# Optimization experiments

Hardware: AMD Instinct MI355X
Metric: run time of the kernel (lower is better)

Reference implementation:

```python
import jax, jax.numpy as jnp
import numpy as np

B, T, N, D = 64, 12, 207, 128
H, ORDER = 8, 2
HID = 2 * D  # mlp_ratio = 2


def _ln(x, g, b, eps=1e-5):
    m = x.mean(-1, keepdims=True)
    v = ((x - m) ** 2).mean(-1, keepdims=True)
    return (x - m) * jax.lax.rsqrt(v + eps) * g + b


def _l2norm(t, eps=1e-12):
    # matches torch.nn.functional.normalize(dim=-1)
    n = jnp.sqrt((t * t).sum(-1, keepdims=True))
    return t / jnp.maximum(n, eps)


def _fast_attn(q, k, v):
    # q, k, v: (B2, L, H, Dh); Performer-style linear attention from FastAttentionLayer.fast_attention
    q = _l2norm(q)
    k = _l2norm(k)
    L = q.shape[1]
    kvs = jnp.einsum('blhm,blhd->bhmd', k, v)
    num = jnp.einsum('bnhm,bhmd->bnhd', q, kvs) + L * v
    ks_sum = k.sum(axis=1)  # (B2, H, Dh)
    den = jnp.einsum('bnhm,bhm->bnh', q, ks_sum)[..., None] + L
    return num / jnp.maximum(den, 1e-5)


def _fast_layer(x, qkv_w, out_w, out_b):
    # x: (B, T, N, D). qkv_bias=False (mask arg), kernel=3 -> out_proj: Linear(2D, D)
    b, t, n, d = x.shape
    dh = d // H
    qkv = x @ qkv_w.T  # (B, T, N, 3D)
    q, k, v = jnp.split(qkv, 3, axis=-1)
    # spatial pass: attend over the N nodes for each (b, t)
    out_s = _fast_attn(q.reshape(b * t, n, H, dh),
                       k.reshape(b * t, n, H, dh),
                       v.reshape(b * t, n, H, dh)).reshape(b, t, n, d)
    # temporal pass: attend over the T steps for each (b, n)
    qt = q.transpose(0, 2, 1, 3).reshape(b * n, t, H, dh)
    kt = k.transpose(0, 2, 1, 3).reshape(b * n, t, H, dh)
    vt = v.transpose(0, 2, 1, 3).reshape(b * n, t, H, dh)
    out_t = _fast_attn(qt, kt, vt).reshape(b, n, t, d).transpose(0, 2, 1, 3)
    return jnp.concatenate([out_s, out_t], -1) @ out_w.T + out_b


def _forward(x, graph, qkv_w, out_w, out_b, pw_w, pw_b,
             fc1_w, fc1_b, fc2_w, fc2_b, ln1_g, ln1_b, ln2_g, ln2_b):
    # GraphPropagate: x_list = [x, graph @ x, ...] (Ks = ORDER hops)
    xs = [x]
    xk = x
    for _ in range(ORDER - 1):
        xk = jnp.einsum('thi,btij->bthj', graph, xk)
        xs.append(xk)
    # per-hop fast attention + zero-init pointwise branch, summed over hops
    agg = jnp.zeros_like(x)
    for i in range(ORDER):
        agg = agg + _fast_layer(xs[i], qkv_w[i], out_w[i], out_b[i]) + xs[i] @ pw_w[i].T + pw_b[i]
    h = _ln(x + agg, ln1_g, ln1_b)
    ff = jax.nn.relu(h @ fc1_w.T + fc1_b) @ fc2_w.T + fc2_b
    return _ln(h + ff, ln2_g, ln2_b)


def setup_inputs() -> dict:
    key = jax.random.key(0)
    ks = jax.random.split(key, 8)
    s = 0.02
    return {
        'x': jax.random.normal(ks[0], (B, T, N, D), jnp.float32),
        'graph': jax.random.uniform(ks[1], (T, N, N), jnp.float32) / N,
        'qkv_w': jax.random.normal(ks[2], (ORDER, 3 * D, D), jnp.float32) * s,
        'out_w': jax.random.normal(ks[3], (ORDER, D, 2 * D), jnp.float32) * s,
        'out_b': jnp.zeros((ORDER, D), jnp.float32),
        'pw_w': jax.random.normal(ks[4], (ORDER, D, D), jnp.float32) * s,
        'pw_b': jnp.zeros((ORDER, D), jnp.float32),
        'fc1_w': jax.random.normal(ks[5], (HID, D), jnp.float32) * s,
        'fc1_b': jnp.zeros((HID,), jnp.float32),
        'fc2_w': jax.random.normal(ks[6], (D, HID), jnp.float32) * s,
        'fc2_b': jnp.zeros((D,), jnp.float32),
        'ln1_g': jnp.ones((D,), jnp.float32),
        'ln1_b': jnp.zeros((D,), jnp.float32),
        'ln2_g': jnp.ones((D,), jnp.float32),
        'ln2_b': jnp.zeros((D,), jnp.float32),
    }


def reference(x, graph, qkv_w, out_w, out_b, pw_w, pw_b,
              fc1_w, fc1_b, fc2_w, fc2_b, ln1_g, ln1_b, ln2_g, ln2_b):
    return _forward(x, graph, qkv_w, out_w, out_b, pw_w, pw_b,
                    fc1_w, fc1_b, fc2_w, fc2_b, ln1_g, ln1_b, ln2_g, ln2_b)
```

## Files before the change

### kernel.cpp

```cpp
#include <hip/hip_runtime.h>
#include <hip/hip_bf16.h>

#define BB 64
#define TT 12
#define NN 207
#define DD 128
#define HH 8
#define DH 16
#define MROWS (BB*TT*NN)
#define KPAD 224
#define AW 768
#define CHB 32
#define CROWS (CHB*TT*NN)

typedef __bf16 bf16x8 __attribute__((ext_vector_type(8)));
typedef __bf16 bf16x4 __attribute__((ext_vector_type(4)));
typedef float  f32x4  __attribute__((ext_vector_type(4)));

__device__ inline float  b2f(__bf16 v){ return (float)v; }
__device__ inline __bf16 f2b(float v){ return (__bf16)v; }
__device__ inline bf16x8 ldfrag(const __bf16* p){ return *reinterpret_cast<const bf16x8*>(p); }

__device__ inline void gload_lds16(const __bf16* g, __bf16* l){
    __builtin_amdgcn_global_load_lds(
        (const __attribute__((address_space(1))) void*)(g),
        (__attribute__((address_space(3))) void*)(l), 16, 0, 0);
}
__device__ inline int swz(int r){ return (r ^ (r>>2)) & 3; }
__device__ inline int pkey(int c){ return (c + (c>>2)) & 3; }

__global__ __launch_bounds__(256) void xcopy_kernel(const float* __restrict__ x, __bf16* __restrict__ abuf)
{
    int nt = gridDim.x*256;
    for (int gIdx = blockIdx.x*256 + threadIdx.x; gIdx < MROWS*16; gIdx += nt) {
        int row = gIdx >> 4, c8 = (gIdx & 15)*8;
        const float* s = x + (size_t)row*DD + c8;
        f32x4 a = *reinterpret_cast<const f32x4*>(s);
        f32x4 b = *reinterpret_cast<const f32x4*>(s+4);
        bf16x8 r;
        #pragma unroll
        for (int i=0;i<4;i++){ r[i] = f2b(a[i]); r[i+4] = f2b(b[i]); }
        *reinterpret_cast<bf16x8*>(abuf + (size_t)row*AW + c8) = r;
    }
}

__global__ __launch_bounds__(256) void prep_misc_kernel(
    const float* __restrict__ graph, const float* __restrict__ qkv_w,
    const float* __restrict__ out_w, const float* __restrict__ out_b,
    const float* __restrict__ pw_w,  const float* __restrict__ pw_b,
    const float* __restrict__ fc1_w, const float* __restrict__ fc2_w,
    __bf16* __restrict__ gpad, __bf16* __restrict__ qkv_wb, __bf16* __restrict__ wcomb,
    __bf16* __restrict__ fc1_wb, __bf16* __restrict__ fc2_wb, float* __restrict__ bias_comb)
{
    int nt = gridDim.x*256;
    int tid = blockIdx.x*256 + threadIdx.x;
    for (int i = tid; i < TT*NN*KPAD; i += nt) {
        int k = i % KPAD, r = i / KPAD;
        gpad[i] = (k < NN) ? f2b(graph[(size_t)r*NN + k]) : f2b(0.f);
    }
    for (int i = tid; i < 2*3*DD*DD; i += nt) qkv_wb[i] = f2b(qkv_w[i]);
    for (int i = tid; i < DD*AW; i += nt) {
        int c = i / AW, j = i % AW;
        float v;
        if      (j < 128) v = pw_w[c*128 + j];
        else if (j < 256) v = pw_w[128*128 + c*128 + (j-128)];
        else if (j < 512) v = out_w[c*256 + (j-256)];
        else              v = out_w[128*256 + c*256 + (j-512)];
        wcomb[i] = f2b(v);
    }
    for (int i = tid; i < 2*DD*DD; i += nt) fc1_wb[i] = f2b(fc1_w[i]);
    for (int i = tid; i < 2*DD*DD; i += nt) fc2_wb[i] = f2b(fc2_w[i]);
    for (int i = tid; i < DD; i += nt)
        bias_comb[i] = pw_b[i] + pw_b[128+i] + out_b[i] + out_b[128+i];
}

__global__ __launch_bounds__(256) void propagate_kernel(const __bf16* __restrict__ gp,
    __bf16* __restrict__ abuf)
{
    int bt   = blockIdx.x;
    int t    = bt % TT;
    int tile = blockIdx.y;
    int lane = threadIdx.x & 63, w = threadIdx.x >> 6;
    int lhi = lane >> 4, llo = lane & 15;
    __shared__ __attribute__((aligned(16))) __bf16 XT[DD][40];
    const __bf16* xbt  = abuf + (size_t)bt*NN*AW;
    const __bf16* grow = gp + (size_t)t*NN*KPAD;
    int rowbase = tile*64 + w*16;
    f32x4 acc[8];
    #pragma unroll
    for (int i=0;i<8;i++) acc[i] = (f32x4){0.f,0.f,0.f,0.f};
    int arow = rowbase + llo; if (arow > NN-1) arow = NN-1;
    for (int k0=0; k0<KPAD; k0+=32) {
        __syncthreads();
        for (int kl = (threadIdx.x>>7); kl < 32; kl += 2) {
            int kk = k0 + kl, c = threadIdx.x & 127;
            __bf16 xb = (kk < NN) ? xbt[(size_t)kk*AW + c] : f2b(0.f);
            XT[c][(((kl>>3) ^ pkey(c))<<3) | (kl&7)] = xb;
        }
        __syncthreads();
        bf16x8 a = ldfrag(grow + (size_t)arow*KPAD + k0 + lhi*8);
        #pragma unroll
        for (int cf=0;cf<8;cf++){
            int row = cf*16+llo;
            bf16x8 b = *reinterpret_cast<const bf16x8*>(&XT[row][(lhi ^ pkey(row))<<3]);
            acc[cf] = __builtin_amdgcn_mfma_f32_16x16x32_bf16(a, b, acc[cf], 0,0,0);
        }
    }
    #pragma unroll
    for (int e=0;e<4;e++){
        int row = rowbase + lhi*4 + e;
        if (row < NN) {
            #pragma unroll
            for (int cf=0;cf<8;cf++)
                abuf[((size_t)bt*NN + row)*AW + DD + cf*16 + llo] = f2b(acc[cf][e]);
        }
    }
}

template<int MODE, bool RELU>
__global__ __launch_bounds__(512) void gemm_kernel(const __bf16* __restrict__ A, size_t lda,
    const __bf16* __restrict__ W, const float* __restrict__ bias,
    void* out, size_t ldc, int K, int mend,
    const __bf16* __restrict__ resid, size_t ldr,
    const float* __restrict__ lng, const float* __restrict__ lnb)
{
    __shared__ __attribute__((aligned(16))) __bf16 lds[3][12288];
    int w = threadIdx.x >> 6, lane = threadIdx.x & 63;
    int lhi = lane >> 4, llo = lane & 15;
    size_t row0 = (size_t)blockIdx.x*256;
    int col0 = blockIdx.y*128;
    int nt = K >> 5;

    int sA0 = (w*2+0)*64 + lane, sA1 = (w*2+1)*64 + lane, sW = w*64 + lane;
    int rA0 = sA0>>2, uA0 = sA0&3, rA1 = sA1>>2, uA1 = sA1&3, rW = sW>>2, uW = sW&3;
    long gr0 = (long)row0 + rA0; if (gr0 >= mend) gr0 = mend-1;
    long gr1 = (long)row0 + rA1; if (gr1 >= mend) gr1 = mend-1;
    const __bf16* gA0 = A + (size_t)gr0*lda + ((uA0 ^ swz(rA0))<<3);
    const __bf16* gA1 = A + (size_t)gr1*lda + ((uA1 ^ swz(rA1))<<3);
    const __bf16* gW  = W + (size_t)(col0 + rW)*K + ((uW ^ swz(rW))<<3);
    __bf16* base0 = &lds[0][0];

    int aoff[2], woff[8];
    #pragma unroll
    for (int rt=0;rt<2;rt++){
        int rl = w*32 + rt*16 + llo;
        aoff[rt] = rl*32 + ((lhi ^ swz(rl))<<3);
    }
    #pragma unroll
    for (int cf=0;cf<8;cf++){
        int wr = cf*16 + llo;
        woff[cf] = 8192 + wr*32 + ((lhi ^ swz(wr))<<3);
    }

    f32x4 acc[2][8];
    #pragma unroll
    for (int i=0;i<2;i++)
        #pragma unroll
        for (int j=0;j<8;j++) acc[i][j] = (f32x4){0.f,0.f,0.f,0.f};

    #define STAGE(buf, tt) { int k0 = (tt)<<5; __bf16* Lw = base0 + (buf)*12288;           \
        gload_lds16(gA0 + k0, Lw + (w*2+0)*512);                                           \
        gload_lds16(gA1 + k0, Lw + (w*2+1)*512);                                           \
        gload_lds16(gW  + k0, Lw + 8192 + w*512); }

    STAGE(0,0); STAGE(1,1); STAGE(2,2);

    int cur = 0;
    for (int t = 0; t < nt; ++t) {
        if (t <= nt-3)      asm volatile("s_waitcnt vmcnt(6)" ::: "memory");
        else if (t == nt-2) asm volatile("s_waitcnt vmcnt(3)" ::: "memory");
        else                asm volatile("s_waitcnt vmcnt(0)" ::: "memory");
        __builtin_amdgcn_s_barrier();
        __builtin_amdgcn_sched_barrier(0);
        const __bf16* Lb = base0 + cur*12288;
        bf16x8 a[2], b[8];
        #pragma unroll
        for (int rt=0;rt<2;rt++) a[rt] = *reinterpret_cast<const bf16x8*>(&Lb[aoff[rt]]);
        #pragma unroll
        for (int cf=0;cf<8;cf++)  b[cf] = *reinterpret_cast<const bf16x8*>(&Lb[woff[cf]]);
        asm volatile("s_waitcnt lgkmcnt(0)" ::: "memory");
        __builtin_amdgcn_sched_barrier(0);
        __builtin_amdgcn_s_barrier();
        if (t+3 < nt) STAGE(cur, t+3);
        #pragma unroll
        for (int rt=0;rt<2;rt++)
            #pragma unroll
            for (int cf=0;cf<8;cf++)
                acc[rt][cf] = __builtin_amdgcn_mfma_f32_16x16x32_bf16(a[rt], b[cf], acc[rt][cf], 0,0,0);
        cur = (cur == 2) ? 0 : cur + 1;
    }
    #undef STAGE

    float bv[8];
    #pragma unroll
    for (int cf=0;cf<8;cf++) bv[cf] = bias ? bias[col0 + cf*16 + llo] : 0.f;

    if (MODE == 0) {
        #pragma unroll
        for (int rt=0;rt<2;rt++) {
            #pragma unroll
            for (int e=0;e<4;e++) {
                size_t row = row0 + (size_t)w*32 + rt*16 + lhi*4 + e;
                if ((long)row >= mend) continue;
                #pragma unroll
                for (int cf=0;cf<8;cf++) {
                    float v = acc[rt][cf][e] + bv[cf];
                    if (RELU) v = fmaxf(v, 0.f);
                    ((__bf16*)out)[row*ldc + col0 + cf*16 + llo] = f2b(v);
                }
            }
        }
    } else {
        float g8[8], b8[8];
        #pragma unroll
        for (int cf=0;cf<8;cf++){ int c = cf*16 + llo; g8[cf] = lng[c]; b8[cf] = lnb[c]; }
        #pragma unroll
        for (int rt=0;rt<2;rt++) {
            #pragma unroll
            for (int e=0;e<4;e++) {
                size_t row = row0 + (size_t)w*32 + rt*16 + lhi*4 + e;
                if ((long)row >= mend) continue;
                float vals[8], s = 0.f, ss = 0.f;
                #pragma unroll
                for (int cf=0;cf<8;cf++) {
                    int c = cf*16 + llo;
                    float r = b2f(resid[row*ldr + c]);
                    float v = acc[rt][cf][e] + bv[cf] + r;
                    vals[cf] = v; s += v; ss += v*v;
                }
                #pragma unroll
                for (int o=1;o<16;o<<=1){ s += __shfl_xor(s,o,64); ss += __shfl_xor(ss,o,64); }
                float mean = s * (1.f/DD);
                float var  = ss * (1.f/DD) - mean*mean;
                float rs   = rsqrtf(var + 1e-5f);
                #pragma unroll
                for (int cf=0;cf<8;cf++) {
                    float v = (vals[cf]-mean)*rs*g8[cf] + b8[cf];
                    ((__bf16*)out)[row*ldc + cf*16 + llo] = f2b(v);
                }
            }
        }
    }
}

template<bool RELU>
__global__ __launch_bounds__(256) void sgemm_k128(const __bf16* __restrict__ A, size_t lda,
    const __bf16* __restrict__ W, const float* __restrict__ bias,
    __bf16* __restrict__ out, size_t ldc, int ngroups)
{
    __shared__ __attribute__((aligned(16))) __bf16 lds[12][2048];
    int w = threadIdx.x >> 6, lane = threadIdx.x & 63;
    int lhi = lane >> 4, llo = lane & 15;
    int col0 = blockIdx.y*128;

    bf16x8 wf[4][8];
    #pragma unroll
    for (int ks=0;ks<4;ks++)
        #pragma unroll
        for (int cf=0;cf<8;cf++)
            wf[ks][cf] = ldfrag(W + (size_t)(col0 + cf*16 + llo)*128 + ks*32 + lhi*8);

    f32x4 bvv[8];
    #pragma unroll
    for (int cf=0;cf<8;cf++){
        if (bias) bvv[cf] = *reinterpret_cast<const f32x4*>(bias + col0 + cf*16 + lhi*4);
        else      bvv[cf] = (f32x4){0.f,0.f,0.f,0.f};
    }

    size_t gsrc[4];
    #pragma unroll
    for (int j=0;j<4;j++){
        int r = j*4 + lhi;
        int u = llo ^ r;
        gsrc[j] = (size_t)r*lda + (size_t)u*8;
    }
    int aoff[4];
    #pragma unroll
    for (int ks=0;ks<4;ks++) aoff[ks] = llo*128 + (((ks<<2)|lhi) ^ llo)*8;

    int gw = blockIdx.x*4 + w, stride = gridDim.x*4;
    int n = (gw < ngroups) ? ((ngroups-1-gw)/stride + 1) : 0;
    __bf16* slab0 = &lds[w*3][0];

    #define SSTAGE(i) { size_t rbase = (size_t)(gw + (size_t)(i)*stride)*16*lda;           \
        __bf16* L = slab0 + ((i)%3)*2048;                                                  \
        gload_lds16(A + rbase + gsrc[0], L);                                               \
        gload_lds16(A + rbase + gsrc[1], L + 512);                                         \
        gload_lds16(A + rbase + gsrc[2], L + 1024);                                        \
        gload_lds16(A + rbase + gsrc[3], L + 1536); }

    if (n > 0) SSTAGE(0);
    if (n > 1) SSTAGE(1);

    for (int i = 0; i < n; ++i) {
        int kept = ((i+1 < n) ? 4 : 0) + ((i >= 2) ? 16 : i*8);
        if      (kept >= 20) asm volatile("s_waitcnt vmcnt(20)" ::: "memory");
        else if (kept == 16) asm volatile("s_waitcnt vmcnt(16)" ::: "memory");
        else if (kept == 12) asm volatile("s_waitcnt vmcnt(12)" ::: "memory");
        else if (kept == 8)  asm volatile("s_waitcnt vmcnt(8)"  ::: "memory");
        else if (kept == 4)  asm volatile("s_waitcnt vmcnt(4)"  ::: "memory");
        else                 asm volatile("s_waitcnt vmcnt(0)"  ::: "memory");

        const __bf16* Ls = slab0 + (i%3)*2048;
        bf16x8 a[4];
        #pragma unroll
        for (int ks=0;ks<4;ks++) a[ks] = *reinterpret_cast<const bf16x8*>(&Ls[aoff[ks]]);

        if (i+2 < n) SSTAGE(i+2);

        f32x4 acc[8];
        #pragma unroll
        for (int cf=0;cf<8;cf++) acc[cf] = (f32x4){0.f,0.f,0.f,0.f};
        #pragma unroll
        for (int ks=0;ks<4;ks++)
            #pragma unroll
            for (int cf=0;cf<8;cf++)
                acc[cf] = __builtin_amdgcn_mfma_f32_16x16x32_bf16(wf[ks][cf], a[ks], acc[cf], 0,0,0);

        size_t grow = (size_t)(gw + (size_t)i*stride)*16 + llo;
        #pragma unroll
        for (int cf=0;cf<8;cf++){
            bf16x4 o;
            #pragma unroll
            for (int e=0;e<4;e++){
                float v = acc[cf][e] + bvv[cf][e];
                if (RELU) v = fmaxf(v, 0.f);
                o[e] = f2b(v);
            }
            *reinterpret_cast<bf16x4*>(out + grow*ldc + col0 + cf*16 + lhi*4) = o;
        }
    }
    #undef SSTAGE
}

__global__ __launch_bounds__(256) void ffn_kernel(const __bf16* __restrict__ h,
    const __bf16* __restrict__ w1, const float* __restrict__ b1,
    const __bf16* __restrict__ w2, const float* __restrict__ b2,
    const float* __restrict__ lng, const float* __restrict__ lnb,
    float* __restrict__ dout)
{
    __shared__ __attribute__((aligned(16))) __bf16 hring[2][4096];
    __shared__ __attribute__((aligned(16))) __bf16 f1b[8192];
    __shared__ float fl2[2][32][4][2];
    int w = threadIdx.x >> 6, lane = threadIdx.x & 63;
    int lhi = lane >> 4, llo = lane & 15;
    size_t row0 = (size_t)blockIdx.x * 64;

    size_t gsrc[2]; int ldst[2];
    #pragma unroll
    for (int j=0;j<2;j++){
        int i = w*64 + lane + 256*j;
        int r = i >> 4, u = i & 15;
        gsrc[j] = (size_t)r*AW + ((u ^ (r & 15)) << 3);
        ldst[j] = (w*64 + 256*j) * 8;
    }
    #define FSTAGE(slot, g) { const __bf16* src = h + (row0 + (size_t)(g)*32)*AW;          \
        gload_lds16(src + gsrc[0], &hring[slot][0] + ldst[0]);                             \
        gload_lds16(src + gsrc[1], &hring[slot][0] + ldst[1]); }

    f32x4 b1v[4], b2v[2], gv[2], bt2[2];
    #pragma unroll
    for (int c4=0;c4<4;c4++) b1v[c4] = *reinterpret_cast<const f32x4*>(b1 + w*64 + c4*16 + lhi*4);
    #pragma unroll
    for (int c2=0;c2<2;c2++){
        b2v[c2] = *reinterpret_cast<const f32x4*>(b2  + w*32 + c2*16 + lhi*4);
        gv[c2]  = *reinterpret_cast<const f32x4*>(lng + w*32 + c2*16 + lhi*4);
        bt2[c2] = *reinterpret_cast<const f32x4*>(lnb + w*32 + c2*16 + lhi*4);
    }

    FSTAGE(0,0); FSTAGE(1,1);

    for (int g = 0; g < 2; ++g) {
        if (g == 0) asm volatile("s_waitcnt vmcnt(2)" ::: "memory");
        else        asm volatile("s_waitcnt vmcnt(0)" ::: "memory");
        __builtin_amdgcn_s_barrier();
        __builtin_amdgcn_sched_barrier(0);
        const __bf16* Hs = &hring[g][0];

        bf16x8 hb[2][4];
        bf16x4 hres[2][2];
        #pragma unroll
        for (int rf=0;rf<2;rf++){
            int r = rf*16 + llo;
            #pragma unroll
            for (int ks=0;ks<4;ks++)
                hb[rf][ks] = *reinterpret_cast<const bf16x8*>(Hs + r*128 + (((ks*4+lhi) ^ llo) << 3));
            #pragma unroll
            for (int cf=0;cf<2;cf++){
                int unit = w*4 + cf*2 + (lhi>>1);
                hres[cf][rf] = *reinterpret_cast<const bf16x4*>(Hs + r*128 + ((unit ^ llo) << 3) + (lhi & 1)*4);
            }
        }
        asm volatile("s_waitcnt lgkmcnt(0)" ::: "memory");
        __builtin_amdgcn_sched_barrier(0);

        f32x4 acc1[4][2];
        #pragma unroll
        for (int i=0;i<4;i++){ acc1[i][0] = (f32x4){0,0,0,0}; acc1[i][1] = (f32x4){0,0,0,0}; }
        #pragma unroll
        for (int ks=0;ks<4;ks++){
            #pragma unroll
            for (int cf2=0;cf2<4;cf2++){
                bf16x8 wfr = ldfrag(w1 + (size_t)(w*64 + cf2*16 + llo)*128 + ks*32 + lhi*8);
                #pragma unroll
                for (int rf=0;rf<2;rf++)
                    acc1[cf2][rf] = __builtin_amdgcn_mfma_f32_16x16x32_bf16(wfr, hb[rf][ks], acc1[cf2][rf], 0,0,0);
            }
        }
        #pragma unroll
        for (int rf=0;rf<2;rf++){
            int r = rf*16 + llo;
            #pragma unroll
            for (int cf2=0;cf2<4;cf2++){
                bf16x4 o;
                #pragma unroll
                for (int e=0;e<4;e++) o[e] = f2b(fmaxf(acc1[cf2][rf][e] + b1v[cf2][e], 0.f));
                int unit = w*8 + cf2*2 + (lhi>>1);
                *reinterpret_cast<bf16x4*>(&f1b[r*256 + ((unit ^ r) << 3) + (lhi&1)*4]) = o;
            }
        }
        asm volatile("s_waitcnt lgkmcnt(0)" ::: "memory");
        __builtin_amdgcn_sched_barrier(0);
        __builtin_amdgcn_s_barrier();

        f32x4 acc2[2][2];
        acc2[0][0]=(f32x4){0,0,0,0}; acc2[0][1]=(f32x4){0,0,0,0};
        acc2[1][0]=(f32x4){0,0,0,0}; acc2[1][1]=(f32x4){0,0,0,0};
        #pragma unroll
        for (int ks2=0;ks2<8;ks2++){
            bf16x8 fb[2];
            #pragma unroll
            for (int rf=0;rf<2;rf++){
                int r = rf*16 + llo;
                fb[rf] = *reinterpret_cast<const bf16x8*>(&f1b[r*256 + (((ks2*4+lhi) ^ r) << 3)]);
            }
            #pragma unroll
            for (int cf=0;cf<2;cf++){
                bf16x8 wfr = ldfrag(w2 + (size_t)(w*32 + cf*16 + llo)*256 + ks2*32 + lhi*8);
                #pragma unroll
                for (int rf=0;rf<2;rf++)
                    acc2[cf][rf] = __builtin_amdgcn_mfma_f32_16x16x32_bf16(wfr, fb[rf], acc2[cf][rf], 0,0,0);
            }
        }

        float vals[2][2][4]; float s[2] = {0.f,0.f}, ss[2] = {0.f,0.f};
        #pragma unroll
        for (int rf=0;rf<2;rf++)
            #pragma unroll
            for (int cf=0;cf<2;cf++)
                #pragma unroll
                for (int e=0;e<4;e++){
                    float v = acc2[cf][rf][e] + b2v[cf][e] + b2f(hres[cf][rf][e]);
                    vals[rf][cf][e] = v; s[rf] += v; ss[rf] += v*v;
                }
        #pragma unroll
        for (int rf=0;rf<2;rf++){
            s[rf]  += __shfl_xor(s[rf],16,64);  s[rf]  += __shfl_xor(s[rf],32,64);
            ss[rf] += __shfl_xor(ss[rf],16,64); ss[rf] += __shfl_xor(ss[rf],32,64);
            if (lhi == 0){ fl2[g][rf*16+llo][w][0] = s[rf]; fl2[g][rf*16+llo][w][1] = ss[rf]; }
        }
        asm volatile("s_waitcnt lgkmcnt(0)" ::: "memory");
        __builtin_amdgcn_s_barrier();
        #pragma unroll
        for (int rf=0;rf<2;rf++){
            int r = rf*16 + llo;
            float S  = fl2[g][r][0][0]+fl2[g][r][1][0]+fl2[g][r][2][0]+fl2[g][r][3][0];
            float SS = fl2[g][r][0][1]+fl2[g][r][1][1]+fl2[g][r][2][1]+fl2[g][r][3][1];
            float mean = S*(1.f/DD), var = SS*(1.f/DD)-mean*mean, rs = rsqrtf(var+1e-5f);
            size_t grow = row0 + (size_t)g*32 + r;
            #pragma unroll
            for (int cf=0;cf<2;cf++){
                f32x4 o;
                #pragma unroll
                for (int e=0;e<4;e++) o[e] = (vals[rf][cf][e]-mean)*rs*gv[cf][e] + bt2[cf][e];
                *reinterpret_cast<f32x4*>(dout + grow*DD + w*32 + cf*16 + lhi*4) = o;
            }
        }
        if (g == 0) __builtin_amdgcn_s_barrier();
    }
    #undef FSTAGE
}

#define ACH 32
#define SBLKS (CHB*TT*4)
__global__ __launch_bounds__(256) void attn_st_kernel(const __bf16* __restrict__ qkv,
    __bf16* __restrict__ outs, __bf16* __restrict__ outt)
{
    __shared__ __attribute__((aligned(16))) char smem[44032];
    int tid = threadIdx.x;
    int bx = blockIdx.x;

    if (bx < SBLKS) {
        int bt = bx >> 2, g = bx & 3;
        const __bf16* base = qkv + (size_t)bt*NN*384 + g*32;
        __bf16 (*qbuf)[40] = (__bf16(*)[40])(smem);
        __bf16 (*vbuf)[40] = (__bf16(*)[40])(smem + 17920);
        __bf16 (*kbuf)[40] = (__bf16(*)[40])(smem + 35840);
        float (*flk)[16][17] = (float(*)[16][17])(smem + 38400);
        float (*fls)[16]     = (float(*)[16])(smem + 42752);
        int wave = tid >> 6, lane = tid & 63;
        int h2 = tid >> 7;
        int dd = tid & 15;
        int oct = ((tid >> 4) & 3) | ((wave & 1) << 2);
        float kvs_col[16]; float ks = 0.f;
        #pragma unroll
        for (int m=0;m<16;m++) kvs_col[m] = 0.f;

        for (int c0 = 0; c0 < NN; c0 += ACH) {
            __syncthreads();
            for (int i = tid; i < ACH*12; i += 256) {
                int r = i/12, u = i%12, seg = u>>2, uu = u&3;
                int nn = c0 + r;
                bf16x8 v8 = (bf16x8){};
                if (nn < NN) v8 = *reinterpret_cast<const bf16x8*>(base + (size_t)nn*384 + seg*128 + uu*8);
                if      (seg == 0) *reinterpret_cast<bf16x8*>(&qbuf[nn][uu*8]) = v8;
                else if (seg == 1) *reinterpret_cast<bf16x8*>(&kbuf[r][uu*8])  = v8;
                else               *reinterpret_cast<bf16x8*>(&vbuf[nn][uu*8]) = v8;
            }
            __syncthreads();
            #pragma unroll
            for (int j=0;j<4;j++){
                int r = oct + 8*j; int nn = c0 + r;
                if (nn >= NN) continue;
                bf16x8 k0 = *reinterpret_cast<const bf16x8*>(&kbuf[r][h2*16]);
                bf16x8 k1 = *reinterpret_cast<const bf16x8*>(&kbuf[r][h2*16+8]);
                float sk = 0.f;
                #pragma unroll
                for (int m=0;m<8;m++){
                    float a0=b2f(k0[m]), a1=b2f(k1[m]); sk += a0*a0 + a1*a1;
                }
                float iv = 1.f/fmaxf(sqrtf(sk), 1e-12f);
                float vv  = b2f(vbuf[nn][h2*16+dd]);
                float kdd = b2f(kbuf[r][h2*16+dd]);
                float t2 = iv*vv;
                #pragma unroll
                for (int m=0;m<8;m++){
                    kvs_col[m]   += b2f(k0[m])*t2;
                    kvs_col[m+8] += b2f(k1[m])*t2;
                }
                ks += kdd*iv;
            }
        }
        #pragma unroll
        for (int m=0;m<16;m++){
            kvs_col[m] += __shfl_xor(kvs_col[m], 16, 64);
            kvs_col[m] += __shfl_xor(kvs_col[m], 32, 64);
        }
        ks += __shfl_xor(ks, 16, 64);
        ks += __shfl_xor(ks, 32, 64);
        if (lane < 16){
            #pragma unroll
            for (int m=0;m<16;m++) flk[wave][m][lane] = kvs_col[m];
            fls[wave][lane] = ks;
        }
        __syncthreads();
        float ksr[16];
        #pragma unroll
        for (int m=0;m<16;m++){
            kvs_col[m] += flk[wave^1][m][dd];
            ksr[m] = fls[h2*2][m] + fls[h2*2+1][m];
        }
        for (int nn = oct; nn < NN; nn += 8) {
            bf16x8 q0 = *reinterpret_cast<const bf16x8*>(&qbuf[nn][h2*16]);
            bf16x8 q1 = *reinterpret_cast<const bf16x8*>(&qbuf[nn][h2*16+8]);
            float sq = 0.f, num = 0.f, den = 0.f;
            #pragma unroll
            for (int m=0;m<8;m++){
                float qm0 = b2f(q0[m]), qm1 = b2f(q1[m]);
                sq  += qm0*qm0 + qm1*qm1;
                num += qm0*kvs_col[m] + qm1*kvs_col[m+8];
                den += qm0*ksr[m]     + qm1*ksr[m+8];
            }
            float iq = 1.f/fmaxf(sqrtf(sq), 1e-12f);
            float vv = b2f(vbuf[nn][h2*16+dd]);
            float o = (num*iq + (float)NN*vv) / fmaxf(den*iq + (float)NN, 1e-5f);
            outs[((size_t)bt*NN + nn)*AW + g*32 + h2*16 + dd] = f2b(o);
        }
    } else {
        int tix = bx - SBLKS;
        int b = tix / 104;
        int nn0 = (tix % 104) * 2;
        __bf16 (*rows)[2][384] = (__bf16(*)[2][384])(smem);
        float (*invq)[TT][8]  = (float(*)[TT][8])(smem + 18432);
        float (*invk2)[TT][8] = (float(*)[TT][8])(smem + 19200);
        for (int i = tid; i < TT*2*48; i += 256) {
            int t = i / 96, rem = i % 96;
            int nl = rem / 48, g = rem % 48;
            int nn = nn0 + nl;
            bf16x8 v8 = (bf16x8){};
            if (nn < NN) v8 = *reinterpret_cast<const bf16x8*>(qkv + ((size_t)(b*TT+t)*NN + nn)*384 + g*8);
            *reinterpret_cast<bf16x8*>(&rows[t][nl][g*8]) = v8;
        }
        __syncthreads();
        if (tid < 192) {
            int hh = tid & 7, t = (tid >> 3) % TT, nl = tid / 96;
            bf16x8 q0 = *reinterpret_cast<const bf16x8*>(&rows[t][nl][hh*16]);
            bf16x8 q1 = *reinterpret_cast<const bf16x8*>(&rows[t][nl][hh*16+8]);
            bf16x8 k0 = *reinterpret_cast<const bf16x8*>(&rows[t][nl][128+hh*16]);
            bf16x8 k1 = *reinterpret_cast<const bf16x8*>(&rows[t][nl][128+hh*16+8]);
            float sq = 0.f, sk = 0.f;
            #pragma unroll
            for (int m=0;m<8;m++){
                float a0=b2f(q0[m]), a1=b2f(q1[m]); sq += a0*a0 + a1*a1;
                float c0v=b2f(k0[m]), c1=b2f(k1[m]); sk += c0v*c0v + c1*c1;
            }
            invq[nl][t][hh]  = 1.f/fmaxf(sqrtf(sq), 1e-12f);
            invk2[nl][t][hh] = 1.f/fmaxf(sqrtf(sk), 1e-12f);
        }
        __syncthreads();
        int dd = tid & 15, h = (tid >> 4) & 7, nl = tid >> 7;
        int nn = nn0 + nl;
        float kvs_col[16], ksum[16];
        #pragma unroll
        for (int m=0;m<16;m++){ kvs_col[m]=0.f; ksum[m]=0.f; }
        #pragma unroll
        for (int t=0;t<TT;t++){
            float iv = invk2[nl][t][h];
            bf16x8 k0 = *reinterpret_cast<const bf16x8*>(&rows[t][nl][128+h*16]);
            bf16x8 k1 = *reinterpret_cast<const bf16x8*>(&rows[t][nl][128+h*16+8]);
            float vv = b2f(rows[t][nl][256+h*16+dd]);
            float t2 = iv*vv;
            #pragma unroll
            for (int m=0;m<8;m++){
                float km0 = b2f(k0[m]), km1 = b2f(k1[m]);
                kvs_col[m]   += km0*t2;  ksum[m]   += km0*iv;
                kvs_col[m+8] += km1*t2;  ksum[m+8] += km1*iv;
            }
        }
        #pragma unroll
        for (int t=0;t<TT;t++){
            float iq = invq[nl][t][h];
            bf16x8 q0 = *reinterpret_cast<const bf16x8*>(&rows[t][nl][h*16]);
            bf16x8 q1 = *reinterpret_cast<const bf16x8*>(&rows[t][nl][h*16+8]);
            float num = 0.f, den = 0.f;
            #pragma unroll
            for (int m=0;m<8;m++){
                float qm0 = b2f(q0[m]), qm1 = b2f(q1[m]);
                num += qm0*kvs_col[m]  + qm1*kvs_col[m+8];
                den += qm0*ksum[m]     + qm1*ksum[m+8];
            }
            float vv = b2f(rows[t][nl][256+h*16+dd]);
            float o = (num*iq + (float)TT*vv) / fmaxf(den*iq + (float)TT, 1e-5f);
            if (nn < NN)
                outt[((size_t)(b*TT+t)*NN + nn)*AW + h*16 + dd] = f2b(o);
        }
    }
}

extern "C" void kernel_launch(void* const* d_in, const int* in_sizes, int n_in,
                              void* d_out, int out_size, void* d_ws, size_t ws_size,
                              hipStream_t stream)
{
    const float* x     = (const float*)d_in[0];
    const float* graph = (const float*)d_in[1];
    const float* qkv_w = (const float*)d_in[2];
    const float* out_w = (const float*)d_in[3];
    const float* out_b = (const float*)d_in[4];
    const float* pw_w  = (const float*)d_in[5];
    const float* pw_b  = (const float*)d_in[6];
    const float* fc1_w = (const float*)d_in[7];
    const float* fc1_b = (const float*)d_in[8];
    const float* fc2_w = (const float*)d_in[9];
    const float* fc2_b = (const float*)d_in[10];
    const float* ln1g  = (const float*)d_in[11];
    const float* ln1b  = (const float*)d_in[12];
    const float* ln2g  = (const float*)d_in[13];
    const float* ln2b  = (const float*)d_in[14];
    (void)in_sizes; (void)n_in; (void)out_size; (void)ws_size;

    char* ws = (char*)d_ws;
    size_t off = 0;
    __bf16* abuf = (__bf16*)(ws + off); off += (size_t)MROWS*AW*2;
    __bf16* qkvc = (__bf16*)(ws + off); off += (size_t)CROWS*3*DD*2;
    __bf16* gpad = (__bf16*)(ws + off); off += (size_t)TT*NN*KPAD*2;
    __bf16* qkv_wb = (__bf16*)(ws + off); off += (size_t)2*3*DD*DD*2;
    __bf16* wcomb  = (__bf16*)(ws + off); off += (size_t)DD*AW*2;
    __bf16* fc1_wb = (__bf16*)(ws + off); off += (size_t)2*DD*DD*2;
    __bf16* fc2_wb = (__bf16*)(ws + off); off += (size_t)2*DD*DD*2;
    float*  bias_comb = (float*)(ws + off); off += DD*4;

    dim3 blk(256), blk512(512);

    xcopy_kernel<<<dim3(4096), blk, 0, stream>>>(x, abuf);
    prep_misc_kernel<<<dim3(1024), blk, 0, stream>>>(graph, qkv_w, out_w, out_b, pw_w, pw_b,
        fc1_w, fc2_w, gpad, qkv_wb, wcomb, fc1_wb, fc2_wb, bias_comb);
    propagate_kernel<<<dim3(BB*TT, 4), blk, 0, stream>>>(gpad, abuf);

    for (int hop = 0; hop < 2; ++hop) {
        for (int c = 0; c < BB/CHB; ++c) {
            size_t rowoff = (size_t)c*CROWS;
            sgemm_k128<false><<<dim3(170, 3), blk, 0, stream>>>(
                abuf + rowoff*AW + hop*DD, (size_t)AW, qkv_wb + (size_t)hop*3*DD*DD, nullptr,
                qkvc, (size_t)(3*DD), CROWS/16);
            attn_st_kernel<<<dim3(SBLKS + CHB*104), blk, 0, stream>>>(
                qkvc, abuf + rowoff*AW + 256 + hop*256, abuf + rowoff*AW + 384 + hop*256);
        }
    }

    gemm_kernel<3,false><<<dim3(MROWS/256, 1), blk512, 0, stream>>>(
        abuf, (size_t)AW, wcomb, bias_comb, (void*)abuf, (size_t)AW, AW, MROWS,
        abuf, (size_t)AW, ln1g, ln1b);
    ffn_kernel<<<dim3(MROWS/64), blk, 0, stream>>>(
        abuf, fc1_wb, fc1_b, fc2_wb, fc2_b, ln2g, ln2b, (float*)d_out);
}
```

Before: 817.8 us.

## Use MFMA for spatial linear-attention KV and output computation

Rewrites the spatial branch of the attention kernel so that K^T V, the k-sum and the q·KV / q·ksum products run as bf16 MFMA instructions instead of scalar FMA loops. Normalized K and V are staged transposed in shared memory per chunk, and the two waves per head alternate chunks and combine their partial sums afterwards. The change adds shared-memory use, an extra barrier per chunk, and rounds KV and ksum to bf16 before the output MFMA, which costs some precision.

```diff
diff --git a/kernel.cpp b/kernel.cpp
--- a/kernel.cpp
+++ b/kernel.cpp
@@ -16,6 +16,7 @@
 typedef __bf16 bf16x8 __attribute__((ext_vector_type(8)));
 typedef __bf16 bf16x4 __attribute__((ext_vector_type(4)));
 typedef float  f32x4  __attribute__((ext_vector_type(4)));
+typedef short  s16x4  __attribute__((ext_vector_type(4)));
 
 __device__ inline float  b2f(__bf16 v){ return (float)v; }
 __device__ inline __bf16 f2b(float v){ return (__bf16)v; }
@@ -486,7 +487,7 @@
 __global__ __launch_bounds__(256) void attn_st_kernel(const __bf16* __restrict__ qkv,
     __bf16* __restrict__ outs, __bf16* __restrict__ outt)
 {
-    __shared__ __attribute__((aligned(16))) char smem[44032];
+    __shared__ __attribute__((aligned(16))) char smem[49664];
     int tid = threadIdx.x;
     int bx = blockIdx.x;
 
@@ -496,17 +497,24 @@
         __bf16 (*qbuf)[40] = (__bf16(*)[40])(smem);
         __bf16 (*vbuf)[40] = (__bf16(*)[40])(smem + 17920);
         __bf16 (*kbuf)[40] = (__bf16(*)[40])(smem + 35840);
-        float (*flk)[16][17] = (float(*)[16][17])(smem + 38400);
-        float (*fls)[16]     = (float(*)[16])(smem + 42752);
+        __bf16 (*khT)[40]  = (__bf16(*)[40])(smem + 38400);
+        __bf16 (*vT)[40]   = (__bf16(*)[40])(smem + 40960);
+        float  (*iqt)[224] = (float(*)[224])(smem + 43520);
+        float*  kvp        = (float*)(smem + 45312);
+        float*  ksp        = (float*)(smem + 49408);
         int wave = tid >> 6, lane = tid & 63;
-        int h2 = tid >> 7;
-        int dd = tid & 15;
-        int oct = ((tid >> 4) & 3) | ((wave & 1) << 2);
-        float kvs_col[16]; float ks = 0.f;
-        #pragma unroll
-        for (int m=0;m<16;m++) kvs_col[m] = 0.f;
-
-        for (int c0 = 0; c0 < NN; c0 += ACH) {
+        int lhi = lane >> 4, llo = lane & 15;
+        int h = wave >> 1;
+        int r8 = tid >> 3, i8 = tid & 7;
+        int thead = i8 >> 2, tm4 = (i8 & 3) * 4;
+
+        f32x4 kvs = (f32x4){0,0,0,0}, ksm = (f32x4){0,0,0,0};
+        bf16x8 ones8;
+        #pragma unroll
+        for (int j=0;j<8;j++) ones8[j] = f2b(1.0f);
+
+        for (int c = 0; c < 7; ++c) {
+            int c0 = c*32;
             __syncthreads();
             for (int i = tid; i < ACH*12; i += 256) {
                 int r = i/12, u = i%12, seg = u>>2, uu = u&3;
@@ -518,63 +526,65 @@
                 else               *reinterpret_cast<bf16x8*>(&vbuf[nn][uu*8]) = v8;
             }
             __syncthreads();
-            #pragma unroll
-            for (int j=0;j<4;j++){
-                int r = oct + 8*j; int nn = c0 + r;
-                if (nn >= NN) continue;
-                bf16x8 k0 = *reinterpret_cast<const bf16x8*>(&kbuf[r][h2*16]);
-                bf16x8 k1 = *reinterpret_cast<const bf16x8*>(&kbuf[r][h2*16+8]);
-                float sk = 0.f;
-                #pragma unroll
-                for (int m=0;m<8;m++){
-                    float a0=b2f(k0[m]), a1=b2f(k1[m]); sk += a0*a0 + a1*a1;
+            {
+                int r = r8, nn = c0 + r8;
+                float kv[4], vv[4];
+                float sk = 0.f, sq = 0.f;
+                #pragma unroll
+                for (int j=0;j<4;j++){
+                    kv[j] = b2f(kbuf[r][thead*16 + tm4 + j]); sk += kv[j]*kv[j];
+                    float qv = b2f(qbuf[nn][thead*16 + tm4 + j]); sq += qv*qv;
+                    vv[j] = b2f(vbuf[nn][thead*16 + tm4 + j]);
                 }
+                sk += __shfl_xor(sk,1,64); sk += __shfl_xor(sk,2,64);
+                sq += __shfl_xor(sq,1,64); sq += __shfl_xor(sq,2,64);
                 float iv = 1.f/fmaxf(sqrtf(sk), 1e-12f);
-                float vv  = b2f(vbuf[nn][h2*16+dd]);
-                float kdd = b2f(kbuf[r][h2*16+dd]);
-                float t2 = iv*vv;
-                #pragma unroll
-                for (int m=0;m<8;m++){
-                    kvs_col[m]   += b2f(k0[m])*t2;
-                    kvs_col[m+8] += b2f(k1[m])*t2;
+                #pragma unroll
+                for (int j=0;j<4;j++){
+                    khT[thead*16 + tm4 + j][r] = f2b(kv[j]*iv);
+                    vT [thead*16 + tm4 + j][r] = f2b(vv[j]);
                 }
-                ks += kdd*iv;
-            }
-        }
-        #pragma unroll
-        for (int m=0;m<16;m++){
-            kvs_col[m] += __shfl_xor(kvs_col[m], 16, 64);
-            kvs_col[m] += __shfl_xor(kvs_col[m], 32, 64);
-        }
-        ks += __shfl_xor(ks, 16, 64);
-        ks += __shfl_xor(ks, 32, 64);
-        if (lane < 16){
-            #pragma unroll
-            for (int m=0;m<16;m++) flk[wave][m][lane] = kvs_col[m];
-            fls[wave][lane] = ks;
+                if ((i8 & 3) == 0) iqt[thead][nn] = 1.f/fmaxf(sqrtf(sq), 1e-12f);
+            }
+            __syncthreads();
+            if ((c & 1) == (wave & 1)) {
+                bf16x8 a = *reinterpret_cast<const bf16x8*>(&khT[h*16 + llo][lhi*8]);
+                bf16x8 b = *reinterpret_cast<const bf16x8*>(&vT [h*16 + llo][lhi*8]);
+                kvs = __builtin_amdgcn_mfma_f32_16x16x32_bf16(a, b, kvs, 0,0,0);
+                ksm = __builtin_amdgcn_mfma_f32_16x16x32_bf16(a, ones8, ksm, 0,0,0);
+            }
+        }
+        #pragma unroll
+        for (int e=0;e<4;e++) kvp[wave*256 + (lhi*4+e)*16 + llo] = kvs[e];
+        if (llo == 0){
+            #pragma unroll
+            for (int e=0;e<4;e++) ksp[wave*16 + lhi*4 + e] = ksm[e];
         }
         __syncthreads();
-        float ksr[16];
-        #pragma unroll
-        for (int m=0;m<16;m++){
-            kvs_col[m] += flk[wave^1][m][dd];
-            ksr[m] = fls[h2*2][m] + fls[h2*2+1][m];
-        }
-        for (int nn = oct; nn < NN; nn += 8) {
-            bf16x8 q0 = *reinterpret_cast<const bf16x8*>(&qbuf[nn][h2*16]);
-            bf16x8 q1 = *reinterpret_cast<const bf16x8*>(&qbuf[nn][h2*16+8]);
-            float sq = 0.f, num = 0.f, den = 0.f;
-            #pragma unroll
-            for (int m=0;m<8;m++){
-                float qm0 = b2f(q0[m]), qm1 = b2f(q1[m]);
-                sq  += qm0*qm0 + qm1*qm1;
-                num += qm0*kvs_col[m] + qm1*kvs_col[m+8];
-                den += qm0*ksr[m]     + qm1*ksr[m+8];
-            }
-            float iq = 1.f/fmaxf(sqrtf(sq), 1e-12f);
-            float vv = b2f(vbuf[nn][h2*16+dd]);
-            float o = (num*iq + (float)NN*vv) / fmaxf(den*iq + (float)NN, 1e-5f);
-            outs[((size_t)bt*NN + nn)*AW + g*32 + h2*16 + dd] = f2b(o);
+        int pw = wave ^ 1;
+        #pragma unroll
+        for (int e=0;e<4;e++){
+            kvs[e] += kvp[pw*256 + (lhi*4+e)*16 + llo];
+            ksm[e] += ksp[pw*16 + lhi*4 + e];
+        }
+        union { bf16x4 b; s16x4 s; } bk, bs;
+        #pragma unroll
+        for (int e=0;e<4;e++){ bk.b[e] = f2b(kvs[e]); bs.b[e] = f2b(ksm[e]); }
+        for (int t = (wave & 1); t < 13; t += 2) {
+            int n0 = t*16;
+            union { bf16x4 b; s16x4 s; } aq;
+            aq.b = *reinterpret_cast<const bf16x4*>(&qbuf[n0 + llo][h*16 + lhi*4]);
+            f32x4 num = __builtin_amdgcn_mfma_f32_16x16x16bf16_1k(aq.s, bk.s, (f32x4){0,0,0,0}, 0,0,0);
+            f32x4 den = __builtin_amdgcn_mfma_f32_16x16x16bf16_1k(aq.s, bs.s, (f32x4){0,0,0,0}, 0,0,0);
+            #pragma unroll
+            for (int e=0;e<4;e++){
+                int n = n0 + lhi*4 + e;
+                if (n >= NN) continue;
+                float iq = iqt[h][n];
+                float vv = b2f(vbuf[n][h*16 + llo]);
+                float o = (num[e]*iq + (float)NN*vv) / fmaxf(den[e]*iq + (float)NN, 1e-5f);
+                outs[((size_t)bt*NN + n)*AW + g*32 + h*16 + llo] = f2b(o);
+            }
         }
     } else {
         int tix = bx - SBLKS;
```

After: 723.5 us. -11.5%, faster.
